# Optimization experiments

Hardware: AMD Instinct MI355X
Metric: run time of the kernel (lower is better)

## Reference

```python
import jax, jax.numpy as jnp
import numpy as np

DIM = 1024
HEADS = 16
DIM_HEAD = 64
INNER = HEADS * DIM_HEAD
LN_EPS = 1e-5


def setup_inputs() -> dict:
    key = jax.random.key(0)
    ks = jax.random.split(key, 6)
    b, n = 2, 2048
    x = jax.random.normal(ks[0], (b, n, DIM), dtype=jnp.float32)
    attn_bias = jax.random.normal(ks[1], (HEADS, n, n), dtype=jnp.float32)
    # learned params
    ln_gamma = jnp.ones((DIM,), dtype=jnp.float32)
    ln_beta = jnp.zeros((DIM,), dtype=jnp.float32)
    w_qkv = jax.random.normal(ks[2], (DIM, 3 * INNER), dtype=jnp.float32) / np.sqrt(DIM)
    w_out = jax.random.normal(ks[3], (INNER, DIM), dtype=jnp.float32) / np.sqrt(INNER)
    return {"x": x, "attn_bias": attn_bias, "ln_gamma": ln_gamma,
            "ln_beta": ln_beta, "w_qkv": w_qkv, "w_out": w_out}


def reference(x, attn_bias, ln_gamma, ln_beta, w_qkv, w_out):
    b, n, _ = x.shape
    scale = DIM_HEAD ** -0.5
    # LayerNorm
    mu = jnp.mean(x, axis=-1, keepdims=True)
    var = jnp.mean(jnp.square(x - mu), axis=-1, keepdims=True)
    xn = (x - mu) * jax.lax.rsqrt(var + LN_EPS) * ln_gamma + ln_beta
    # QKV projection: [b, n, 3*inner]
    qkv = xn @ w_qkv
    q, k, v = jnp.split(qkv, 3, axis=-1)
    # [b, n, inner] -> [b, h, n, d]
    split_heads = lambda t: t.reshape(b, n, HEADS, DIM_HEAD).transpose(0, 2, 1, 3)
    q, k, v = split_heads(q) * scale, split_heads(k), split_heads(v)
    sim = jnp.einsum('bhid,bhjd->bhij', q, k)
    sim = sim + attn_bias[None]  # broadcast over batch
    mask_value = -jnp.finfo(sim.dtype).max
    causal = jnp.triu(jnp.ones((n, n), dtype=bool), k=1)
    sim = jnp.where(causal, mask_value, sim)
    attn = jax.nn.softmax(sim, axis=-1)
    out = jnp.einsum('bhij,bhjd->bhid', attn, v)
    out = out.transpose(0, 2, 1, 3).reshape(b, n, INNER)
    return out @ w_out
```

## Files before the change

kernel.cpp:

```cpp
#include <hip/hip_runtime.h>
#include <hip/hip_bf16.h>
#include <math.h>

typedef unsigned short u16;
typedef __attribute__((ext_vector_type(8))) __bf16 bf16x8;
typedef __attribute__((ext_vector_type(4))) float f32x4;

static __device__ __forceinline__ u16 f2bf(float f) {
    unsigned int u = __builtin_bit_cast(unsigned int, f);
    u += 0x7fffu + ((u >> 16) & 1u);
    return (u16)(u >> 16);
}

__global__ __launch_bounds__(256) void ln_kernel(
    const float* __restrict__ x, const float* __restrict__ g,
    const float* __restrict__ bta, u16* __restrict__ xn)
{
    const int row = blockIdx.x;
    const int tid = threadIdx.x;
    const float4 v = *(const float4*)&x[(size_t)row * 1024 + tid * 4];
    float s  = v.x + v.y + v.z + v.w;
    float s2 = v.x * v.x + v.y * v.y + v.z * v.z + v.w * v.w;
    #pragma unroll
    for (int off = 32; off; off >>= 1) {
        s  += __shfl_xor(s,  off);
        s2 += __shfl_xor(s2, off);
    }
    __shared__ float red[8];
    if ((tid & 63) == 0) { red[tid >> 6] = s; red[4 + (tid >> 6)] = s2; }
    __syncthreads();
    s  = red[0] + red[1] + red[2] + red[3];
    s2 = red[4] + red[5] + red[6] + red[7];
    const float mean = s * (1.0f / 1024.0f);
    const float var  = s2 * (1.0f / 1024.0f) - mean * mean;
    const float rstd = rsqrtf(var + 1e-5f);
    const float4 gg = *(const float4*)&g[tid * 4];
    const float4 bb = *(const float4*)&bta[tid * 4];
    ushort4 o;
    o.x = f2bf((v.x - mean) * rstd * gg.x + bb.x);
    o.y = f2bf((v.y - mean) * rstd * gg.y + bb.y);
    o.z = f2bf((v.z - mean) * rstd * gg.z + bb.z);
    o.w = f2bf((v.w - mean) * rstd * gg.w + bb.w);
    *(ushort4*)&xn[(size_t)row * 1024 + tid * 4] = o;
}

__global__ __launch_bounds__(256) void transpose_w(
    const float* __restrict__ in, u16* __restrict__ outT, int K, int N)
{
    const int k0 = blockIdx.x * 64, n0 = blockIdx.y * 64;
    const int tid = threadIdx.x;
    __shared__ u16 tile[64][72];
    #pragma unroll
    for (int i = 0; i < 4; ++i) {
        int c = tid + i * 256;
        int kr = c >> 4, nc = (c & 15) * 4;
        float4 v = *(const float4*)&in[(size_t)(k0 + kr) * N + n0 + nc];
        tile[nc + 0][kr] = f2bf(v.x);
        tile[nc + 1][kr] = f2bf(v.y);
        tile[nc + 2][kr] = f2bf(v.z);
        tile[nc + 3][kr] = f2bf(v.w);
    }
    __syncthreads();
    #pragma unroll
    for (int i = 0; i < 4; ++i) {
        int c = tid + i * 256;
        int nr = c >> 4, kc = (c & 15) * 4;
        ushort4 w = *(const ushort4*)&tile[nr][kc];
        *(ushort4*)&outT[(size_t)(n0 + nr) * K + k0 + kc] = w;
    }
}

__global__ __launch_bounds__(256) void transpose_v_kernel(
    const u16* __restrict__ V, u16* __restrict__ Vt)
{
    const int bh = blockIdx.y;
    const int n0 = blockIdx.x * 64;
    const int tid = threadIdx.x;
    __shared__ u16 t[64][72];
    #pragma unroll
    for (int i = 0; i < 2; ++i) {
        int c = tid + (i << 8);
        int nr = c >> 3, dc = (c & 7) * 8;
        int4 v4 = *(const int4*)&V[((size_t)bh * 2048 + n0 + nr) * 64 + dc];
        union { int4 v; u16 u[8]; } uu; uu.v = v4;
        #pragma unroll
        for (int j = 0; j < 8; ++j) t[dc + j][nr] = uu.u[j];
    }
    __syncthreads();
    #pragma unroll
    for (int i = 0; i < 2; ++i) {
        int c = tid + (i << 8);
        int d = c >> 3, nn = (c & 7) * 8;
        int4 v4 = *(const int4*)&t[d][nn];
        *(int4*)&Vt[((size_t)bh * 64 + d) * 2048 + n0 + nn] = v4;
    }
}

template <int EPI>
__global__ __launch_bounds__(256) void gemm_bf16_k(
    const u16* __restrict__ A, const u16* __restrict__ Bt,
    int M, int N, int K,
    float* __restrict__ Cf,
    u16* __restrict__ Qo, u16* __restrict__ Ko, u16* __restrict__ Vo)
{
    __shared__ u16 lds[2][8192];
    const int tid = threadIdx.x;
    const int lane = tid & 63, w = tid >> 6;
    const int l15 = lane & 15, l4 = lane >> 4;
    const int wm = w & 1, wn = w >> 1;
    const int n0 = blockIdx.x * 128, m0 = blockIdx.y * 128;

    auto stage = [&](int buf, int kt) {
        const u16* Ab = A + (size_t)m0 * K + kt * 32;
        const u16* Bb = Bt + (size_t)n0 * K + kt * 32;
        #pragma unroll
        for (int i = 0; i < 2; ++i) {
            int c = tid + (i << 8);
            int r = c >> 2, ke = (c & 3) * 8;
            __builtin_amdgcn_global_load_lds(
                (const __attribute__((address_space(1))) void*)(Ab + (size_t)r * K + ke),
                (__attribute__((address_space(3))) void*)(&lds[buf][0] + c * 8), 16, 0, 0);
            __builtin_amdgcn_global_load_lds(
                (const __attribute__((address_space(1))) void*)(Bb + (size_t)r * K + ke),
                (__attribute__((address_space(3))) void*)(&lds[buf][4096] + c * 8), 16, 0, 0);
        }
    };

    f32x4 acc[4][4];
    #pragma unroll
    for (int mf = 0; mf < 4; ++mf)
        #pragma unroll
        for (int nf = 0; nf < 4; ++nf)
            acc[mf][nf] = f32x4{0.f, 0.f, 0.f, 0.f};

    const int NT = K >> 5;
    stage(0, 0);
    __syncthreads();
    for (int kt = 0; kt < NT; ++kt) {
        const int buf = kt & 1;
        if (kt + 1 < NT) stage(buf ^ 1, kt + 1);
        const u16* Ab = &lds[buf][0];
        const u16* Bb = &lds[buf][4096];
        bf16x8 af[4], bfv[4];
        #pragma unroll
        for (int mf = 0; mf < 4; ++mf)
            af[mf] = *(const bf16x8*)(Ab + (wm * 64 + mf * 16 + l15) * 32 + l4 * 8);
        #pragma unroll
        for (int nf = 0; nf < 4; ++nf)
            bfv[nf] = *(const bf16x8*)(Bb + (wn * 64 + nf * 16 + l15) * 32 + l4 * 8);
        #pragma unroll
        for (int mf = 0; mf < 4; ++mf)
            #pragma unroll
            for (int nf = 0; nf < 4; ++nf)
                acc[mf][nf] = __builtin_amdgcn_mfma_f32_16x16x32_bf16(
                    af[mf], bfv[nf], acc[mf][nf], 0, 0, 0);
        __syncthreads();
    }

    #pragma unroll
    for (int mf = 0; mf < 4; ++mf) {
        #pragma unroll
        for (int nf = 0; nf < 4; ++nf) {
            #pragma unroll
            for (int r = 0; r < 4; ++r) {
                const int row = m0 + wm * 64 + mf * 16 + l4 * 4 + r;
                const int col = n0 + wn * 64 + nf * 16 + l15;
                const float v = acc[mf][nf][r];
                if (EPI == 1) {
                    Cf[(size_t)row * N + col] = v;
                } else {
                    const int t = col >> 10, rem = col & 1023;
                    const int h = rem >> 6, d = rem & 63;
                    const int b = row >> 11, nn = row & 2047;
                    const size_t idx = ((size_t)((b * 16 + h) * 2048 + nn)) * 64 + d;
                    if (t == 0)      Qo[idx] = f2bf(v * 0.125f);
                    else if (t == 1) Ko[idx] = f2bf(v);
                    else             Vo[idx] = f2bf(v);
                }
            }
        }
    }
}

__global__ __launch_bounds__(512, 2) void attn_kernel(
    const u16* __restrict__ Q, const u16* __restrict__ Kmat,
    const u16* __restrict__ Vt, const float* __restrict__ bias,
    u16* __restrict__ att)
{
    const int hb = blockIdx.x;
    const int h = hb >> 1, b = hb & 1;
    const int bh = b * 16 + h;
    const int y = blockIdx.y;
    const int qb = (y < 8) ? y : 23 - y;
    const int q0 = qb << 7;
    const int tid = threadIdx.x;
    const int w = tid >> 6, lane = tid & 63;
    const int l15 = lane & 15, l4 = lane >> 4;

    __shared__ u16 K_lds[2][64][72];
    __shared__ u16 V_lds[2][64][72];
    __shared__ u16 P_lds[8][16][72];

    const int qrow_a = q0 + w * 16 + l15;
    bf16x8 qa[2];
    #pragma unroll
    for (int ks = 0; ks < 2; ++ks)
        qa[ks] = *(const bf16x8*)(Q + ((size_t)bh * 2048 + qrow_a) * 64 + ks * 32 + l4 * 8);

    f32x4 acc_o[4];
    #pragma unroll
    for (int nf = 0; nf < 4; ++nf) acc_o[nf] = f32x4{0.f, 0.f, 0.f, 0.f};
    float m_r[4], l_r[4];
    #pragma unroll
    for (int r = 0; r < 4; ++r) { m_r[r] = -INFINITY; l_r[r] = 0.f; }

    const int qrow_c = q0 + w * 16 + l4 * 4;
    const int qlim = q0 + w * 16 + 15;
    const float* biasrow = bias + (size_t)h * 2048 * 2048;

    const int rr_s = tid >> 3, pp_s = (tid & 7) * 8;
    int4 kreg, vreg;
    auto issue_loads = [&](int j0n) {
        kreg = *(const int4*)&Kmat[((size_t)bh * 2048 + j0n + rr_s) * 64 + pp_s];
        vreg = *(const int4*)&Vt[((size_t)bh * 64 + rr_s) * 2048 + j0n + pp_s];
    };
    auto load_bias = [&](int j0n, float (&dst)[4][4]) {
        #pragma unroll
        for (int nf = 0; nf < 4; ++nf)
            #pragma unroll
            for (int r = 0; r < 4; ++r)
                dst[nf][r] = biasrow[(size_t)(qrow_c + r) * 2048 + j0n + nf * 16 + l15];
    };

    const int NT = 2 * qb + 2;
    float bregA[4][4], bregB[4][4];

    issue_loads(0);
    load_bias(0, bregA);

    auto tile_step = [&](int jt, float (&bcur)[4][4], float (&bnext)[4][4]) {
        const int j0 = jt << 6;
        const int buf = jt & 1;
        *(int4*)&K_lds[buf][rr_s][pp_s] = kreg;
        *(int4*)&V_lds[buf][rr_s][pp_s] = vreg;
        if (jt + 1 < NT) {
            issue_loads((jt + 1) << 6);
            if (((jt + 1) << 6) <= qlim) load_bias((jt + 1) << 6, bnext);
        }
        __builtin_amdgcn_sched_barrier(0);
        asm volatile("s_waitcnt lgkmcnt(0)" ::: "memory");
        __builtin_amdgcn_s_barrier();
        __builtin_amdgcn_sched_barrier(0);

        if (j0 <= qlim) {
            f32x4 s[4];
            #pragma unroll
            for (int nf = 0; nf < 4; ++nf) s[nf] = f32x4{0.f, 0.f, 0.f, 0.f};
            __builtin_amdgcn_s_setprio(1);
            #pragma unroll
            for (int ks = 0; ks < 2; ++ks)
                #pragma unroll
                for (int nf = 0; nf < 4; ++nf) {
                    bf16x8 kb = *(const bf16x8*)&K_lds[buf][nf * 16 + l15][ks * 32 + l4 * 8];
                    s[nf] = __builtin_amdgcn_mfma_f32_16x16x32_bf16(qa[ks], kb, s[nf], 0, 0, 0);
                }
            __builtin_amdgcn_s_setprio(0);

            float p[4][4];
            if (j0 + 63 > q0 + w * 16) {
                #pragma unroll
                for (int nf = 0; nf < 4; ++nf) {
                    const int col = j0 + nf * 16 + l15;
                    #pragma unroll
                    for (int r = 0; r < 4; ++r) {
                        const int qr = qrow_c + r;
                        float v = s[nf][r] + bcur[nf][r];
                        p[nf][r] = (col > qr) ? -1e30f : v;
                    }
                }
            } else {
                #pragma unroll
                for (int nf = 0; nf < 4; ++nf)
                    #pragma unroll
                    for (int r = 0; r < 4; ++r)
                        p[nf][r] = s[nf][r] + bcur[nf][r];
            }

            float mt[4];
            #pragma unroll
            for (int r = 0; r < 4; ++r)
                mt[r] = fmaxf(fmaxf(p[0][r], p[1][r]), fmaxf(p[2][r], p[3][r]));
            int need = 0;
            #pragma unroll
            for (int r = 0; r < 4; ++r) need |= (mt[r] > m_r[r] + 8.0f);
            if (__any(need)) {
                #pragma unroll
                for (int off = 1; off < 16; off <<= 1)
                    #pragma unroll
                    for (int r = 0; r < 4; ++r) mt[r] = fmaxf(mt[r], __shfl_xor(mt[r], off));
                #pragma unroll
                for (int r = 0; r < 4; ++r) {
                    const float mn = fmaxf(m_r[r], mt[r]);
                    const float alpha = __expf(m_r[r] - mn);
                    m_r[r] = mn;
                    l_r[r] *= alpha;
                    #pragma unroll
                    for (int nf = 0; nf < 4; ++nf) acc_o[nf][r] *= alpha;
                }
            }

            float ps[4] = {0.f, 0.f, 0.f, 0.f};
            #pragma unroll
            for (int nf = 0; nf < 4; ++nf)
                #pragma unroll
                for (int r = 0; r < 4; ++r) {
                    const float e = __expf(p[nf][r] - m_r[r]);
                    ps[r] += e;
                    P_lds[w][l4 * 4 + r][nf * 16 + l15] = f2bf(e);
                }
            #pragma unroll
            for (int off = 1; off < 16; off <<= 1)
                #pragma unroll
                for (int r = 0; r < 4; ++r) ps[r] += __shfl_xor(ps[r], off);
            #pragma unroll
            for (int r = 0; r < 4; ++r) l_r[r] += ps[r];

            __builtin_amdgcn_s_setprio(1);
            #pragma unroll
            for (int ks = 0; ks < 2; ++ks) {
                bf16x8 pa = *(const bf16x8*)&P_lds[w][l15][ks * 32 + l4 * 8];
                #pragma unroll
                for (int nf = 0; nf < 4; ++nf) {
                    bf16x8 vb = *(const bf16x8*)&V_lds[buf][nf * 16 + l15][ks * 32 + l4 * 8];
                    acc_o[nf] = __builtin_amdgcn_mfma_f32_16x16x32_bf16(pa, vb, acc_o[nf], 0, 0, 0);
                }
            }
            __builtin_amdgcn_s_setprio(0);
        }
    };

    for (int jt = 0; jt < NT; jt += 2) {
        tile_step(jt,     bregA, bregB);
        tile_step(jt + 1, bregB, bregA);
    }

    #pragma unroll
    for (int nf = 0; nf < 4; ++nf)
        #pragma unroll
        for (int r = 0; r < 4; ++r) {
            const int qr = qrow_c + r;
            const float o = acc_o[nf][r] / l_r[r];
            att[((size_t)b * 2048 + qr) * 1024 + h * 64 + nf * 16 + l15] = f2bf(o);
        }
}

extern "C" void kernel_launch(void* const* d_in, const int* in_sizes, int n_in,
                              void* d_out, int out_size, void* d_ws, size_t ws_size,
                              hipStream_t stream) {
    const float* x     = (const float*)d_in[0];
    const float* bias  = (const float*)d_in[1];
    const float* gamma = (const float*)d_in[2];
    const float* beta_ = (const float*)d_in[3];
    const float* wqkv  = (const float*)d_in[4];
    const float* wout  = (const float*)d_in[5];
    float* out = (float*)d_out;

    char* ws = (char*)d_ws;
    u16* xn     = (u16*)(ws + 0);
    u16* wqkvT  = (u16*)(ws + 8388608);
    u16* woutT  = (u16*)(ws + 14680064);
    u16* Qb     = (u16*)(ws + 16777216);
    u16* Kb     = (u16*)(ws + 25165824);
    u16* Vb     = (u16*)(ws + 33554432);
    u16* Vtb    = (u16*)(ws + 41943040);
    u16* attb   = xn;

    ln_kernel<<<4096, 256, 0, stream>>>(x, gamma, beta_, xn);
    transpose_w<<<dim3(16, 48), 256, 0, stream>>>(wqkv, wqkvT, 1024, 3072);
    transpose_w<<<dim3(16, 16), 256, 0, stream>>>(wout, woutT, 1024, 1024);
    gemm_bf16_k<0><<<dim3(24, 32), 256, 0, stream>>>(xn, wqkvT, 4096, 3072, 1024,
                                                     nullptr, Qb, Kb, Vb);
    transpose_v_kernel<<<dim3(32, 32), 256, 0, stream>>>(Vb, Vtb);
    attn_kernel<<<dim3(32, 16), 512, 0, stream>>>(Qb, Kb, Vtb, bias, attb);
    gemm_bf16_k<1><<<dim3(8, 32), 256, 0, stream>>>(attb, woutT, 4096, 1024, 1024,
                                                    out, nullptr, nullptr, nullptr);
}
```

Before: 147.3 us.

## Transpose attention MFMA operands so each lane owns one query row

Swaps the A/B operands of both MFMAs so the accumulator is transposed and each lane holds one full query row across columns. Bias then loads as contiguous float4 per lane, the softmax max and sum need only two cross-lane shuffles with scalar running stats, and P and the output are written as packed ushort4. It also raises launch bounds to 4 waves per SIMD, pads LDS rows to 76, and prefetches bias two tiles ahead into the buffer just consumed. The higher occupancy target may force register spills or cut latency hiding, and the new LDS padding may change bank-conflict behaviour.

```diff
diff --git a/kernel.cpp b/kernel.cpp
--- a/kernel.cpp
+++ b/kernel.cpp
@@ -182,7 +182,7 @@
     }
 }
 
-__global__ __launch_bounds__(512, 2) void attn_kernel(
+__global__ __launch_bounds__(512, 4) void attn_kernel(
     const u16* __restrict__ Q, const u16* __restrict__ Kmat,
     const u16* __restrict__ Vt, const float* __restrict__ bias,
     u16* __restrict__ att)
@@ -197,26 +197,24 @@
     const int w = tid >> 6, lane = tid & 63;
     const int l15 = lane & 15, l4 = lane >> 4;
 
-    __shared__ u16 K_lds[2][64][72];
-    __shared__ u16 V_lds[2][64][72];
-    __shared__ u16 P_lds[8][16][72];
-
-    const int qrow_a = q0 + w * 16 + l15;
+    __shared__ u16 K_lds[2][64][76];
+    __shared__ u16 V_lds[2][64][76];
+    __shared__ u16 P_lds[8][16][76];
+
+    const int qrow = q0 + w * 16 + l15;
+    const int qlim = q0 + w * 16 + 15;
+
     bf16x8 qa[2];
     #pragma unroll
     for (int ks = 0; ks < 2; ++ks)
-        qa[ks] = *(const bf16x8*)(Q + ((size_t)bh * 2048 + qrow_a) * 64 + ks * 32 + l4 * 8);
-
-    f32x4 acc_o[4];
-    #pragma unroll
-    for (int nf = 0; nf < 4; ++nf) acc_o[nf] = f32x4{0.f, 0.f, 0.f, 0.f};
-    float m_r[4], l_r[4];
-    #pragma unroll
-    for (int r = 0; r < 4; ++r) { m_r[r] = -INFINITY; l_r[r] = 0.f; }
-
-    const int qrow_c = q0 + w * 16 + l4 * 4;
-    const int qlim = q0 + w * 16 + 15;
-    const float* biasrow = bias + (size_t)h * 2048 * 2048;
+        qa[ks] = *(const bf16x8*)(Q + ((size_t)bh * 2048 + qrow) * 64 + ks * 32 + l4 * 8);
+
+    f32x4 acc[4];
+    #pragma unroll
+    for (int nf = 0; nf < 4; ++nf) acc[nf] = f32x4{0.f, 0.f, 0.f, 0.f};
+    float m_r = -INFINITY, l_r = 0.f;
+
+    const float* biasq = bias + (size_t)h * 2048 * 2048 + (size_t)qrow * 2048;
 
     const int rr_s = tid >> 3, pp_s = (tid & 7) * 8;
     int4 kreg, vreg;
@@ -224,29 +222,25 @@
         kreg = *(const int4*)&Kmat[((size_t)bh * 2048 + j0n + rr_s) * 64 + pp_s];
         vreg = *(const int4*)&Vt[((size_t)bh * 64 + rr_s) * 2048 + j0n + pp_s];
     };
-    auto load_bias = [&](int j0n, float (&dst)[4][4]) {
+    auto load_bias = [&](int j0n, float4 (&dst)[4]) {
         #pragma unroll
         for (int nf = 0; nf < 4; ++nf)
-            #pragma unroll
-            for (int r = 0; r < 4; ++r)
-                dst[nf][r] = biasrow[(size_t)(qrow_c + r) * 2048 + j0n + nf * 16 + l15];
+            dst[nf] = *(const float4*)&biasq[j0n + nf * 16 + l4 * 4];
     };
 
     const int NT = 2 * qb + 2;
-    float bregA[4][4], bregB[4][4];
+    float4 bregA[4], bregB[4];
 
     issue_loads(0);
     load_bias(0, bregA);
-
-    auto tile_step = [&](int jt, float (&bcur)[4][4], float (&bnext)[4][4]) {
+    if (64 <= qlim && NT > 1) load_bias(64, bregB);
+
+    auto tile_step = [&](int jt, float4 (&bcur)[4]) {
         const int j0 = jt << 6;
         const int buf = jt & 1;
         *(int4*)&K_lds[buf][rr_s][pp_s] = kreg;
         *(int4*)&V_lds[buf][rr_s][pp_s] = vreg;
-        if (jt + 1 < NT) {
-            issue_loads((jt + 1) << 6);
-            if (((jt + 1) << 6) <= qlim) load_bias((jt + 1) << 6, bnext);
-        }
+        if (jt + 1 < NT) issue_loads((jt + 1) << 6);
         __builtin_amdgcn_sched_barrier(0);
         asm volatile("s_waitcnt lgkmcnt(0)" ::: "memory");
         __builtin_amdgcn_s_barrier();
@@ -262,20 +256,18 @@
                 #pragma unroll
                 for (int nf = 0; nf < 4; ++nf) {
                     bf16x8 kb = *(const bf16x8*)&K_lds[buf][nf * 16 + l15][ks * 32 + l4 * 8];
-                    s[nf] = __builtin_amdgcn_mfma_f32_16x16x32_bf16(qa[ks], kb, s[nf], 0, 0, 0);
+                    s[nf] = __builtin_amdgcn_mfma_f32_16x16x32_bf16(kb, qa[ks], s[nf], 0, 0, 0);
                 }
             __builtin_amdgcn_s_setprio(0);
 
-            float p[4][4];
             if (j0 + 63 > q0 + w * 16) {
                 #pragma unroll
                 for (int nf = 0; nf < 4; ++nf) {
-                    const int col = j0 + nf * 16 + l15;
+                    const int col0 = j0 + nf * 16 + l4 * 4;
                     #pragma unroll
                     for (int r = 0; r < 4; ++r) {
-                        const int qr = qrow_c + r;
-                        float v = s[nf][r] + bcur[nf][r];
-                        p[nf][r] = (col > qr) ? -1e30f : v;
+                        const float v = s[nf][r] + ((const float*)&bcur[nf])[r];
+                        s[nf][r] = (col0 + r > qrow) ? -1e30f : v;
                     }
                 }
             } else {
@@ -283,47 +275,43 @@
                 for (int nf = 0; nf < 4; ++nf)
                     #pragma unroll
                     for (int r = 0; r < 4; ++r)
-                        p[nf][r] = s[nf][r] + bcur[nf][r];
-            }
-
-            float mt[4];
-            #pragma unroll
-            for (int r = 0; r < 4; ++r)
-                mt[r] = fmaxf(fmaxf(p[0][r], p[1][r]), fmaxf(p[2][r], p[3][r]));
-            int need = 0;
-            #pragma unroll
-            for (int r = 0; r < 4; ++r) need |= (mt[r] > m_r[r] + 8.0f);
-            if (__any(need)) {
-                #pragma unroll
-                for (int off = 1; off < 16; off <<= 1)
+                        s[nf][r] += ((const float*)&bcur[nf])[r];
+            }
+            if (jt + 2 < NT && ((jt + 2) << 6) <= qlim)
+                load_bias((jt + 2) << 6, bcur);
+
+            float mt = fmaxf(fmaxf(fmaxf(s[0][0], s[0][1]), fmaxf(s[0][2], s[0][3])),
+                             fmaxf(fmaxf(s[1][0], s[1][1]), fmaxf(s[1][2], s[1][3])));
+            mt = fmaxf(mt, fmaxf(fmaxf(fmaxf(s[2][0], s[2][1]), fmaxf(s[2][2], s[2][3])),
+                                 fmaxf(fmaxf(s[3][0], s[3][1]), fmaxf(s[3][2], s[3][3]))));
+            mt = fmaxf(mt, __shfl_xor(mt, 16));
+            mt = fmaxf(mt, __shfl_xor(mt, 32));
+            if (__any(mt > m_r + 8.0f)) {
+                const float mn = fmaxf(m_r, mt);
+                const float alpha = __expf(m_r - mn);
+                m_r = mn;
+                l_r *= alpha;
+                #pragma unroll
+                for (int nf = 0; nf < 4; ++nf)
                     #pragma unroll
-                    for (int r = 0; r < 4; ++r) mt[r] = fmaxf(mt[r], __shfl_xor(mt[r], off));
+                    for (int r = 0; r < 4; ++r) acc[nf][r] *= alpha;
+            }
+
+            float ps = 0.f;
+            #pragma unroll
+            for (int nf = 0; nf < 4; ++nf) {
+                union { ushort4 v; u16 e[4]; } pw;
                 #pragma unroll
                 for (int r = 0; r < 4; ++r) {
-                    const float mn = fmaxf(m_r[r], mt[r]);
-                    const float alpha = __expf(m_r[r] - mn);
-                    m_r[r] = mn;
-                    l_r[r] *= alpha;
-                    #pragma unroll
-                    for (int nf = 0; nf < 4; ++nf) acc_o[nf][r] *= alpha;
-                }
-            }
-
-            float ps[4] = {0.f, 0.f, 0.f, 0.f};
-            #pragma unroll
-            for (int nf = 0; nf < 4; ++nf)
-                #pragma unroll
-                for (int r = 0; r < 4; ++r) {
-                    const float e = __expf(p[nf][r] - m_r[r]);
-                    ps[r] += e;
-                    P_lds[w][l4 * 4 + r][nf * 16 + l15] = f2bf(e);
-                }
-            #pragma unroll
-            for (int off = 1; off < 16; off <<= 1)
-                #pragma unroll
-                for (int r = 0; r < 4; ++r) ps[r] += __shfl_xor(ps[r], off);
-            #pragma unroll
-            for (int r = 0; r < 4; ++r) l_r[r] += ps[r];
+                    const float e = __expf(s[nf][r] - m_r);
+                    ps += e;
+                    pw.e[r] = f2bf(e);
+                }
+                *(ushort4*)&P_lds[w][l15][nf * 16 + l4 * 4] = pw.v;
+            }
+            ps += __shfl_xor(ps, 16);
+            ps += __shfl_xor(ps, 32);
+            l_r += ps;
 
             __builtin_amdgcn_s_setprio(1);
             #pragma unroll
@@ -332,7 +320,7 @@
                 #pragma unroll
                 for (int nf = 0; nf < 4; ++nf) {
                     bf16x8 vb = *(const bf16x8*)&V_lds[buf][nf * 16 + l15][ks * 32 + l4 * 8];
-                    acc_o[nf] = __builtin_amdgcn_mfma_f32_16x16x32_bf16(pa, vb, acc_o[nf], 0, 0, 0);
+                    acc[nf] = __builtin_amdgcn_mfma_f32_16x16x32_bf16(vb, pa, acc[nf], 0, 0, 0);
                 }
             }
             __builtin_amdgcn_s_setprio(0);
@@ -340,18 +328,18 @@
     };
 
     for (int jt = 0; jt < NT; jt += 2) {
-        tile_step(jt,     bregA, bregB);
-        tile_step(jt + 1, bregB, bregA);
-    }
-
-    #pragma unroll
-    for (int nf = 0; nf < 4; ++nf)
-        #pragma unroll
-        for (int r = 0; r < 4; ++r) {
-            const int qr = qrow_c + r;
-            const float o = acc_o[nf][r] / l_r[r];
-            att[((size_t)b * 2048 + qr) * 1024 + h * 64 + nf * 16 + l15] = f2bf(o);
-        }
+        tile_step(jt,     bregA);
+        tile_step(jt + 1, bregB);
+    }
+
+    const float inv = 1.0f / l_r;
+    #pragma unroll
+    for (int nf = 0; nf < 4; ++nf) {
+        union { ushort4 v; u16 e[4]; } o;
+        #pragma unroll
+        for (int r = 0; r < 4; ++r) o.e[r] = f2bf(acc[nf][r] * inv);
+        *(ushort4*)&att[((size_t)b * 2048 + qrow) * 1024 + h * 64 + nf * 16 + l4 * 4] = o.v;
+    }
 }
 
 extern "C" void kernel_launch(void* const* d_in, const int* in_sizes, int n_in,
```

New measurement: 151.5 us. 2.8% more time.
